# Performance work log

Hardware: AMD Instinct MI355X
Metric: run time of the kernel (lower is better)

## Reference

```python
import jax, jax.numpy as jnp
import numpy as np

N_STATE = 512
M_IN = 64
P_OUT = 64
BATCH = 32
SEQ = 2048


def setup_inputs() -> dict:
    key = jax.random.key(0)
    k1, k2, k3, k4, k5 = jax.random.split(key, 5)
    u = jax.random.normal(k1, (BATCH, SEQ, M_IN), dtype=jnp.float32)
    # CompanionParam init: a ~ randn * 0.01 (keeps companion matrix stable, near shift matrix)
    a = jax.random.normal(k2, (N_STATE,), dtype=jnp.float32) * 0.01
    B = jax.random.normal(k3, (N_STATE, M_IN), dtype=jnp.float32) * 0.05
    C = jax.random.normal(k4, (P_OUT, N_STATE), dtype=jnp.float32) * 0.05
    D = jax.random.normal(k5, (P_OUT, M_IN), dtype=jnp.float32) * 0.05
    return {"u": u, "a": a, "B": B, "C": C, "D": D}


def companion_matrix(a):
    # A[i+1, i] = 1 on subdiagonal; last column = -flip(a)  (matches CompanionParam.matrix)
    n = a.shape[0]
    idx = jnp.arange(n - 1)
    A = jnp.zeros((n, n), dtype=a.dtype)
    A = A.at[idx + 1, idx].set(1.0)
    A = A.at[:, n - 1].set(-a[::-1])
    return A


def reference(u, a, B, C, D):
    # LTI SSM recurrence: x_t = A x_{t-1} + B u_t ; y_t = C x_t + D u_t
    A = companion_matrix(a)  # (n, n)
    batch, T, m = u.shape
    n = a.shape[0]
    u_t = jnp.transpose(u, (1, 0, 2))  # (T, batch, m)
    Bu = jnp.einsum('tbm,nm->tbn', u_t, B)  # precompute input drive (T, batch, n)

    def step(x, bu):
        x_new = x @ A.T + bu  # (batch, n)
        return x_new, x_new

    x0 = jnp.zeros((batch, n), dtype=u.dtype)
    _, xs = jax.lax.scan(step, x0, Bu)  # xs: (T, batch, n)
    ys = jnp.einsum('tbn,pn->tbp', xs, C) + jnp.einsum('tbm,pm->tbp', u_t, D)
    return jnp.transpose(ys, (1, 0, 2))  # (batch, T, p)
```

## Files before the change

### kernel.cpp

```cpp
#include <hip/hip_runtime.h>

#define SEQ  2048
#define NB   32
#define NS   512
#define MI   64
#define PO   64
#define TB   64
#define NTB  32
#define CH   64
#define NCH  8
#define LDU  72
#define LDD  68
#define SG_LDA 72

typedef __attribute__((ext_vector_type(8))) __bf16 bf16x8;
typedef __attribute__((ext_vector_type(4))) float  floatx4;

__device__ inline unsigned short f2bf(float f) {
    unsigned u = __builtin_bit_cast(unsigned, f);
    u += 0x7fff + ((u >> 16) & 1);
    return (unsigned short)(u >> 16);
}

__global__ void __launch_bounds__(256) prep_all_kernel(
    const float* __restrict__ u, const float* __restrict__ B,
    const float* __restrict__ C, const float* __restrict__ D,
    const float* __restrict__ a,
    unsigned short* __restrict__ ubf, unsigned short* __restrict__ BflatT,
    unsigned short* __restrict__ Bws, unsigned short* __restrict__ Cws,
    unsigned short* __restrict__ Dws, unsigned short* __restrict__ qT) {
    __shared__ float a_ext[1024];
    const int bx = blockIdx.x, tid = threadIdx.x;
    if (bx < 2048) {
        const size_t base = ((size_t)bx * 256 + tid) * 8;
        float4 f0 = *(const float4*)(u + base);
        float4 f1 = *(const float4*)(u + base + 4);
        unsigned short tmp[8];
        tmp[0] = f2bf(f0.x); tmp[1] = f2bf(f0.y); tmp[2] = f2bf(f0.z); tmp[3] = f2bf(f0.w);
        tmp[4] = f2bf(f1.x); tmp[5] = f2bf(f1.y); tmp[6] = f2bf(f1.z); tmp[7] = f2bf(f1.w);
        *(uint4*)(ubf + base) = *(uint4*)&tmp[0];
    } else if (bx < 2560) {
        const int i = bx - 2048;
        for (int r = 0; r < 2; ++r) {
            const int id = tid + r * 256;
            const int j = id >> 3, q8 = (id & 7) * 8;
            unsigned short tmp[8];
            if (i >= j) {
                const float4 f0 = *(const float4*)(B + (size_t)(i - j) * MI + q8);
                const float4 f1 = *(const float4*)(B + (size_t)(i - j) * MI + q8 + 4);
                tmp[0] = f2bf(f0.x); tmp[1] = f2bf(f0.y); tmp[2] = f2bf(f0.z); tmp[3] = f2bf(f0.w);
                tmp[4] = f2bf(f1.x); tmp[5] = f2bf(f1.y); tmp[6] = f2bf(f1.z); tmp[7] = f2bf(f1.w);
            } else {
#pragma unroll
                for (int z = 0; z < 8; ++z) tmp[z] = 0;
            }
            *(uint4*)(BflatT + (size_t)i * 4096 + j * 64 + q8) = *(uint4*)&tmp[0];
        }
    } else if (bx < 2624) {
        const int p = bx - 2560;
        for (int x = tid; x < 1024; x += 256) a_ext[x] = (x < NS) ? a[x] : 0.f;
        __syncthreads();
        const int j0 = tid, j1 = tid + 256;
        float acc0 = 0.f, acc1 = 0.f;
        const float4* crow = (const float4*)(C + (size_t)p * NS);
        for (int i4 = 0; i4 < NS / 4; ++i4) {
            const float4 cv = crow[i4];
            const int base = 511 - i4 * 4;
            acc0 += cv.x * a_ext[base + j0]     + cv.y * a_ext[base - 1 + j0] +
                    cv.z * a_ext[base - 2 + j0] + cv.w * a_ext[base - 3 + j0];
            acc1 += cv.x * a_ext[base + j1]     + cv.y * a_ext[base - 1 + j1] +
                    cv.z * a_ext[base - 2 + j1] + cv.w * a_ext[base - 3 + j1];
        }
        qT[(size_t)p * NS + j0] = f2bf(acc0);
        qT[(size_t)p * NS + j1] = f2bf(acc1);
    } else {
        const int idx = (bx - 2624) * 256 + tid;
        const int nB = NS * MI, nC = PO * NS, nD = PO * MI;
        if (idx < nB) Bws[idx] = f2bf(B[idx]);
        else if (idx < nB + nC) Cws[idx - nB] = f2bf(C[idx - nB]);
        else if (idx < nB + nC + nD) Dws[idx - nB - nC] = f2bf(D[idx - nB - nC]);
    }
}

__global__ void __launch_bounds__(256) sgemm_kernel(const unsigned short* __restrict__ ubf,
                                                    const unsigned short* __restrict__ BflatT,
                                                    float* __restrict__ Sbuf) {
    __shared__ unsigned short A_l[4 * 64 * SG_LDA];
    __shared__ unsigned short U_l[4 * 32 * SG_LDA];
    const int ib = blockIdx.x, b = blockIdx.y;
    const int tid = threadIdx.x, lane = tid & 63, w = tid >> 6;
    const int row16 = lane & 15, quad = lane >> 4;
    const int i0 = ib * 64;
    floatx4 acc[2];
#pragma unroll
    for (int ns = 0; ns < 2; ++ns) acc[ns] = (floatx4){0.f, 0.f, 0.f, 0.f};

    for (int jg = 0; jg < 16; ++jg) {
#pragma unroll
        for (int r = 0; r < 8; ++r) {
            const int id = tid + r * 256;
            const int row = id >> 5;
            const int jj = (id >> 3) & 3, q8 = (id & 7) * 8;
            const int j = jg * 4 + jj;
            *(uint4*)&A_l[(jj * 64 + row) * SG_LDA + q8] =
                *(const uint4*)(BflatT + (size_t)(i0 + row) * 4096 + j * 64 + q8);
        }
#pragma unroll
        for (int r = 0; r < 4; ++r) {
            const int id = tid + r * 256;
            const int n = id >> 5;
            const int jj = (id >> 3) & 3, q8 = (id & 7) * 8;
            const int j = jg * 4 + jj;
            *(uint4*)&U_l[(jj * 32 + n) * SG_LDA + q8] =
                *(const uint4*)(ubf + ((size_t)b * SEQ + n * 64 + 63 - j) * MI + q8);
        }
        __syncthreads();
#pragma unroll
        for (int jj = 0; jj < 4; ++jj) {
#pragma unroll
            for (int mk = 0; mk < 2; ++mk) {
                const bf16x8 av = *(const bf16x8*)
                    &A_l[(jj * 64 + w * 16 + row16) * SG_LDA + mk * 32 + quad * 8];
#pragma unroll
                for (int ns = 0; ns < 2; ++ns) {
                    const bf16x8 bv = *(const bf16x8*)
                        &U_l[(jj * 32 + ns * 16 + row16) * SG_LDA + mk * 32 + quad * 8];
                    acc[ns] = __builtin_amdgcn_mfma_f32_16x16x32_bf16(av, bv, acc[ns], 0, 0, 0);
                }
            }
        }
        __syncthreads();
    }
#pragma unroll
    for (int ns = 0; ns < 2; ++ns) {
        const int n = ns * 16 + row16;
        float* dst = Sbuf + ((size_t)b * NTB + n) * NS + i0 + w * 16 + quad * 4;
        *(floatx4*)dst = acc[ns];
    }
}

__global__ void __launch_bounds__(1024) scan_himp_kernel(const float* __restrict__ Sbuf,
                                                         float* __restrict__ Rbuf,
                                                         const float* __restrict__ a,
                                                         float* __restrict__ hbuf) {
    __shared__ __align__(16) char smem[24576];
    const int tid = threadIdx.x;
    if (blockIdx.x < NB) {
        const int b = blockIdx.x;
        const float4* S4 = (const float4*)(Sbuf + (size_t)b * NTB * NS);
        float4* R4 = (float4*)(Rbuf + (size_t)b * NTB * NS);
        for (int o = tid; o < NTB * NS / 4; o += 1024) {
            const int k = o >> 7;
            const int i4 = o & 127;
            float4 acc = make_float4(0.f, 0.f, 0.f, 0.f);
#pragma unroll
            for (int m = 0; m < 8; ++m) {
                if (m <= k - 1 && i4 >= 16 * m) {
                    const float4 s = S4[(k - 1 - m) * 128 + i4 - 16 * m];
                    acc.x += s.x; acc.y += s.y; acc.z += s.z; acc.w += s.w;
                }
            }
            R4[o] = acc;
        }
    } else {
        float* a_l     = (float*)smem;
        float* h_ext   = (float*)(smem + 2560);
        float* part    = (float*)(smem + 12800);
        float* rhs_ext = (float*)(smem + 20992);
        const int kk = tid & 63, grp = tid >> 6;

        for (int x = tid; x < 640; x += 1024) a_l[x] = (x < NS) ? a[x] : 0.f;
        for (int x = tid; x < 640; x += 1024) h_ext[x] = 0.f;
        if (tid < 256) rhs_ext[tid] = 0.f;
        __syncthreads();

        float aw[34];
#pragma unroll
        for (int i = 0; i < 34; ++i) aw[i] = a_l[2 * kk + grp * 32 + i];

        if (tid < 64) {
            if (tid == 0) h_ext[512] = 1.f;
            float acc = (tid >= 1) ? a_l[tid - 1] : 0.f;
            for (int s = 1; s < 64; ++s) {
                const float hs = -__shfl(acc, s);
                if (tid == s) h_ext[512 + s] = hs;
                const float av = a_l[(tid > s) ? (tid - 1 - s) : 0];
                acc += (tid > s) ? av * hs : 0.f;
            }
        }
        __syncthreads();

        int t0 = 64;
        while (t0 < SEQ) {
            float acc0 = 0.f, acc1 = 0.f;
#pragma unroll
            for (int m = 0; m < 8; ++m) {
                const float4 hv = *(const float4*)&h_ext[512 + t0 - grp * 32 - 4 - 4 * m];
                acc0 += aw[4 * m + 0] * hv.w + aw[4 * m + 1] * hv.z +
                        aw[4 * m + 2] * hv.y + aw[4 * m + 3] * hv.x;
                acc1 += aw[4 * m + 1] * hv.w + aw[4 * m + 2] * hv.z +
                        aw[4 * m + 3] * hv.y + aw[4 * m + 4] * hv.x;
            }
            *(float2*)&part[grp * 128 + 2 * kk] = make_float2(acc0, acc1);
            __syncthreads();
            if (tid < 128) {
                float r = 0.f;
#pragma unroll
                for (int g = 0; g < 16; ++g) r += part[g * 128 + tid];
                rhs_ext[128 + tid] = -r;
            }
            __syncthreads();
            {
                const int g = tid >> 7, out = tid & 127;
                const int k0 = g * 16;
                float s = 0.f;
#pragma unroll
                for (int k4 = 0; k4 < 4; ++k4) {
                    const float4 h4 = *(const float4*)&h_ext[512 + k0 + 4 * k4];
                    const int base = 128 + out - k0 - 4 * k4;
                    s += h4.x * rhs_ext[base]     + h4.y * rhs_ext[base - 1] +
                         h4.z * rhs_ext[base - 2] + h4.w * rhs_ext[base - 3];
                }
                part[g * 128 + out] = s;
            }
            __syncthreads();
            if (tid < 128) {
                float r = 0.f;
#pragma unroll
                for (int g = 0; g < 8; ++g) r += part[g * 128 + tid];
                h_ext[512 + t0 + tid] = r;
            }
            __syncthreads();
            t0 += (t0 == 64) ? 64 : 128;
        }
        for (int i = tid; i < SEQ; i += 1024) hbuf[i] = h_ext[512 + i];
    }
}

__global__ void __launch_bounds__(256, 4) ytile_kernel(
    const unsigned short* __restrict__ ubf, const unsigned short* __restrict__ Bws,
    const unsigned short* __restrict__ Cws, const unsigned short* __restrict__ Dws,
    const float* __restrict__ Rbuf, float* __restrict__ fbuf, float* __restrict__ y) {
    __shared__ __align__(16) float buDiag[TB * LDD];
    __shared__ __align__(16) unsigned short Gb[TB * LDU];

    const int blk = blockIdx.x, b = blockIdx.y;
    const int t0 = blk * TB;
    const int tid = threadIdx.x;
    const int lane = tid & 63, w = tid >> 6;
    const int row16 = lane & 15, quad = lane >> 4;
    const size_t rbase = ((size_t)b * NTB + blk) * NS;

    const int dd = lane >> 2, seg = lane & 3;
    const int d  = w * 16 + dd;
    const int tsplit = 63 - d, gseg = tsplit >> 4, jsplit = tsplit & 15;
    const int qb = lane & 60;

    float sA = (d >= 1) ? Rbuf[rbase + d - 1] : 0.f;
    float cB = 0.f;

    floatx4 accY[4];
#pragma unroll
    for (int nt = 0; nt < 4; ++nt) accY[nt] = (floatx4){0.f, 0.f, 0.f, 0.f};

    bf16x8 ufr0[4], ufr1[4];
#pragma unroll
    for (int nt = 0; nt < 4; ++nt) {
        const size_t ub = ((size_t)b * SEQ + t0 + nt * 16 + row16) * MI;
        ufr0[nt] = *(const bf16x8*)(ubf + ub + quad * 8);
        ufr1[nt] = *(const bf16x8*)(ubf + ub + 32 + quad * 8);
    }

    for (int ch = 0; ch < NCH; ++ch) {
        float sA_next = 0.f;
        if (ch + 1 < NCH) sA_next = Rbuf[rbase + (ch + 1) * 64 + d - 1];

        const bf16x8 bf0 = *(const bf16x8*)(Bws + (size_t)(ch * CH + w * 16 + row16) * MI + quad * 8);
        const bf16x8 bf1 = *(const bf16x8*)(Bws + (size_t)(ch * CH + w * 16 + row16) * MI + 32 + quad * 8);
        const bf16x8 cf0 = *(const bf16x8*)(Cws + (size_t)(w * 16 + row16) * NS + ch * CH + quad * 8);
        const bf16x8 cf1 = *(const bf16x8*)(Cws + (size_t)(w * 16 + row16) * NS + ch * CH + 32 + quad * 8);

#pragma unroll
        for (int nt = 0; nt < 4; ++nt) {
            floatx4 dacc = {0.f, 0.f, 0.f, 0.f};
            dacc = __builtin_amdgcn_mfma_f32_16x16x32_bf16(bf0, ufr0[nt], dacc, 0, 0, 0);
            dacc = __builtin_amdgcn_mfma_f32_16x16x32_bf16(bf1, ufr1[nt], dacc, 0, 0, 0);
            const int t = nt * 16 + row16;
            const int ibase = w * 16 + quad * 4;
#pragma unroll
            for (int r = 0; r < 4; ++r) {
                const int dscat = (ibase + r - t) & 63;
                buDiag[dscat * LDD + t] = dacc[r];
            }
        }
        __syncthreads();

        {
            const float* rowp = &buDiag[d * LDD + seg * 16];
            const float4 v0 = *(const float4*)(rowp + 0);
            const float4 v1 = *(const float4*)(rowp + 4);
            const float4 v2 = *(const float4*)(rowp + 8);
            const float4 v3 = *(const float4*)(rowp + 12);
            float pv[16];
            pv[0]  = v0.x;          pv[1]  = pv[0]  + v0.y;
            pv[2]  = pv[1]  + v0.z; pv[3]  = pv[2]  + v0.w;
            pv[4]  = pv[3]  + v1.x; pv[5]  = pv[4]  + v1.y;
            pv[6]  = pv[5]  + v1.z; pv[7]  = pv[6]  + v1.w;
            pv[8]  = pv[7]  + v2.x; pv[9]  = pv[8]  + v2.y;
            pv[10] = pv[9]  + v2.z; pv[11] = pv[10] + v2.w;
            pv[12] = pv[11] + v3.x; pv[13] = pv[12] + v3.y;
            pv[14] = pv[13] + v3.z; pv[15] = pv[14] + v3.w;
            const float total = pv[15];
            const float tq0 = __shfl(total, qb + 0);
            const float tq1 = __shfl(total, qb + 1);
            const float tq2 = __shfl(total, qb + 2);
            const float off = (seg > 0 ? tq0 : 0.f) + (seg > 1 ? tq1 : 0.f) +
                              (seg > 2 ? tq2 : 0.f);
            float plocal = pv[0];
#pragma unroll
            for (int j = 1; j < 16; ++j) plocal = (j == jsplit) ? pv[j] : plocal;
            const float Ps = __shfl(off + plocal, qb + gseg);
            const float exitv = sA + Ps;
            const float baseLo = sA, baseHi = cB - Ps;
#pragma unroll
            for (int j = 0; j < 16; ++j) {
                const int t = seg * 16 + j;
                const float outv = ((t <= tsplit) ? baseLo : baseHi) + off + pv[j];
                Gb[t * LDU + ((d + t) & 63)] = f2bf(outv);
            }
            if (ch == NCH - 1) {
                if (seg == 0) fbuf[(size_t)b * SEQ + t0 + tsplit] = exitv;
            }
            cB = exitv;
            sA = sA_next;
        }
        __syncthreads();

#pragma unroll
        for (int nt = 0; nt < 4; ++nt) {
            const int t = nt * 16 + row16;
            bf16x8 g0 = *(const bf16x8*)&Gb[t * LDU + quad * 8];
            bf16x8 g1 = *(const bf16x8*)&Gb[t * LDU + 32 + quad * 8];
            accY[nt] = __builtin_amdgcn_mfma_f32_16x16x32_bf16(cf0, g0, accY[nt], 0, 0, 0);
            accY[nt] = __builtin_amdgcn_mfma_f32_16x16x32_bf16(cf1, g1, accY[nt], 0, 0, 0);
        }
    }

    const bf16x8 df0 = *(const bf16x8*)(Dws + (size_t)(w * 16 + row16) * MI + quad * 8);
    const bf16x8 df1 = *(const bf16x8*)(Dws + (size_t)(w * 16 + row16) * MI + 32 + quad * 8);
#pragma unroll
    for (int nt = 0; nt < 4; ++nt) {
        const int t = nt * 16 + row16;
        accY[nt] = __builtin_amdgcn_mfma_f32_16x16x32_bf16(df0, ufr0[nt], accY[nt], 0, 0, 0);
        accY[nt] = __builtin_amdgcn_mfma_f32_16x16x32_bf16(df1, ufr1[nt], accY[nt], 0, 0, 0);
        const int p0 = w * 16 + quad * 4;
        *(floatx4*)(y + ((size_t)b * SEQ + t0 + t) * PO + p0) = accY[nt];
    }
}

__global__ void __launch_bounds__(256) sconv_kernel(const float* __restrict__ fbuf,
                                                    const float* __restrict__ hbuf,
                                                    float* __restrict__ sbuf) {
    __shared__ __align__(16) float f_l[64 + SEQ];
    __shared__ __align__(16) float h_lc[SEQ + 8];
    __shared__ __align__(16) float part[16][TB];
    const int blk = blockIdx.x, b = blockIdx.y, tid = threadIdx.x;
    const int t0 = blk * TB;
    const int len = t0 + TB;
    {
        const float4* fs = (const float4*)(fbuf + (size_t)b * SEQ);
        const float4* hs = (const float4*)hbuf;
        float4* f4 = (float4*)f_l;
        float4* h4p = (float4*)h_lc;
        if (tid < 16) f4[tid] = make_float4(0.f, 0.f, 0.f, 0.f);
        for (int i = tid; i < len / 4; i += 256) f4[16 + i] = fs[i];
        const int nh4 = len / 4 + 2;
        for (int i = tid; i < nh4; i += 256)
            h4p[i] = (i < SEQ / 4) ? hs[i] : make_float4(0.f, 0.f, 0.f, 0.f);
    }
    __syncthreads();
    const int o4 = (tid & 15) * 4, grp = tid >> 4;
    const int tb4 = t0 + o4;
    float a0 = 0.f, a1 = 0.f, a2 = 0.f, a3 = 0.f;
    for (int j4 = grp * 4; j4 <= tb4 + 3; j4 += 64) {
        const float4 hv = *(const float4*)&h_lc[j4];
        const int A = tb4 - j4;
        const float4 q0 = *(const float4*)&f_l[60 + A];
        const float4 q1 = *(const float4*)&f_l[64 + A];
        a0 += hv.x * q1.x + hv.y * q0.w + hv.z * q0.z + hv.w * q0.y;
        a1 += hv.x * q1.y + hv.y * q1.x + hv.z * q0.w + hv.w * q0.z;
        a2 += hv.x * q1.z + hv.y * q1.y + hv.z * q1.x + hv.w * q0.w;
        a3 += hv.x * q1.w + hv.y * q1.z + hv.z * q1.y + hv.w * q1.x;
    }
    *(float4*)&part[grp][o4] = make_float4(a0, a1, a2, a3);
    __syncthreads();
    if (tid < TB) {
        float r = 0.f;
#pragma unroll
        for (int g = 0; g < 16; ++g) r += part[g][tid];
        sbuf[(size_t)b * SEQ + t0 + tid] = r;
    }
}

__global__ void __launch_bounds__(256) corr_kernel(
    const float* __restrict__ sbuf, const unsigned short* __restrict__ qT,
    float* __restrict__ y) {
    __shared__ float s_l[NS + TB];
    __shared__ unsigned short Sw[2][TB * LDU];
    const int blk = blockIdx.x, b = blockIdx.y, tid = threadIdx.x;
    const int t0 = blk * TB;
    const int lane = tid & 63, w = tid >> 6;
    const int row16 = lane & 15, quad = lane >> 4;
    for (int idx = tid; idx < NS + TB; idx += 256) {
        const int t = t0 - NS + idx;
        s_l[idx] = (t >= 0) ? sbuf[(size_t)b * SEQ + t] : 0.f;
    }
    floatx4 acc[4];
#pragma unroll
    for (int nt = 0; nt < 4; ++nt) acc[nt] = (floatx4){0.f, 0.f, 0.f, 0.f};
    __syncthreads();

    for (int ch = 0; ch < NCH; ++ch) {
        const int buf = ch & 1;
        const bf16x8 qf0 = *(const bf16x8*)(qT + (size_t)(w * 16 + row16) * NS + ch * CH + quad * 8);
        const bf16x8 qf1 = *(const bf16x8*)(qT + (size_t)(w * 16 + row16) * NS + ch * CH + 32 + quad * 8);
        {
            const int r = tid >> 2, c0 = (tid & 3) * 16;
            unsigned short tmp[16];
            const int base = 511 + r - ch * CH - c0;
#pragma unroll
            for (int jj = 0; jj < 16; ++jj) tmp[jj] = f2bf(s_l[base - jj]);
            *(uint4*)&Sw[buf][r * LDU + c0]     = *(uint4*)&tmp[0];
            *(uint4*)&Sw[buf][r * LDU + c0 + 8] = *(uint4*)&tmp[8];
        }
        __syncthreads();
#pragma unroll
        for (int nt = 0; nt < 4; ++nt) {
            const int t = nt * 16 + row16;
            bf16x8 s0 = *(const bf16x8*)&Sw[buf][t * LDU + quad * 8];
            bf16x8 s1 = *(const bf16x8*)&Sw[buf][t * LDU + 32 + quad * 8];
            acc[nt] = __builtin_amdgcn_mfma_f32_16x16x32_bf16(qf0, s0, acc[nt], 0, 0, 0);
            acc[nt] = __builtin_amdgcn_mfma_f32_16x16x32_bf16(qf1, s1, acc[nt], 0, 0, 0);
        }
    }
#pragma unroll
    for (int nt = 0; nt < 4; ++nt) {
        const int t = nt * 16 + row16;
        const int p0 = w * 16 + quad * 4;
        float* yp = y + ((size_t)b * SEQ + t0 + t) * PO + p0;
        floatx4 old = *(const floatx4*)yp;
        *(floatx4*)yp = old - acc[nt];
    }
}

extern "C" void kernel_launch(void* const* d_in, const int* in_sizes, int n_in,
                              void* d_out, int out_size, void* d_ws,
                              size_t ws_size, hipStream_t stream) {
    const float* u  = (const float*)d_in[0];
    const float* a  = (const float*)d_in[1];
    const float* B  = (const float*)d_in[2];
    const float* Cm = (const float*)d_in[3];
    const float* Dm = (const float*)d_in[4];
    float* y = (float*)d_out;

    char* ws = (char*)d_ws;
    unsigned short* Bws = (unsigned short*)ws;                  ws += NS * MI * 2;
    unsigned short* Cws = (unsigned short*)ws;                  ws += PO * NS * 2;
    unsigned short* Dws = (unsigned short*)ws;                  ws += PO * MI * 2;
    unsigned short* qTw = (unsigned short*)ws;                  ws += PO * NS * 2;
    unsigned short* ubf = (unsigned short*)ws;                  ws += (size_t)NB * SEQ * MI * 2;
    unsigned short* Bft = (unsigned short*)ws;                  ws += (size_t)NS * 4096 * 2;
    float* Sbuf = (float*)ws;                                   ws += (size_t)NB * NTB * NS * 4;
    float* Rbuf = (float*)ws;                                   ws += (size_t)NB * NTB * NS * 4;
    float* fbuf = (float*)ws;                                   ws += (size_t)NB * SEQ * 4;
    float* sbuf = (float*)ws;                                   ws += (size_t)NB * SEQ * 4;
    float* hbuf = (float*)ws;

    prep_all_kernel<<<dim3(2896), dim3(256), 0, stream>>>(
        u, B, Cm, Dm, a, ubf, Bft, Bws, Cws, Dws, qTw);
    sgemm_kernel<<<dim3(8, 32), dim3(256), 0, stream>>>(ubf, Bft, Sbuf);
    scan_himp_kernel<<<dim3(NB + 1), dim3(1024), 0, stream>>>(Sbuf, Rbuf, a, hbuf);
    ytile_kernel<<<dim3(NTB, NB), dim3(256), 0, stream>>>(
        ubf, Bws, Cws, Dws, Rbuf, fbuf, y);
    sconv_kernel<<<dim3(NTB, NB), dim3(256), 0, stream>>>(fbuf, hbuf, sbuf);
    corr_kernel<<<dim3(NTB, NB), dim3(256), 0, stream>>>(sbuf, qTw, y);
}
```

Before: 204.0 us.

## Fold scan kernel into prep and ytile, drop Rbuf round trip

The h-impulse recurrence moves into an extra 1024-thread block of the prep kernel, so it runs alongside the conversions, and prep switches to 1024-thread blocks. The Rbuf prefix-sum pass is dropped: each ytile block now builds its own seed vector in shared memory from Sbuf. This removes one kernel launch and the Rbuf global write and read. The corr kernel now stores s as bf16 in shared memory, converting once instead of on every reuse. In exchange, the h-scan block now shares a launch with many short blocks and could lengthen the prep kernel's tail, and ytile takes on redundant seed summation.

```diff
diff --git a/kernel.cpp b/kernel.cpp
--- a/kernel.cpp
+++ b/kernel.cpp
@@ -22,63 +22,132 @@
     return (unsigned short)(u >> 16);
 }
 
-__global__ void __launch_bounds__(256) prep_all_kernel(
+__global__ void __launch_bounds__(1024) prep_all_kernel(
     const float* __restrict__ u, const float* __restrict__ B,
     const float* __restrict__ C, const float* __restrict__ D,
     const float* __restrict__ a,
     unsigned short* __restrict__ ubf, unsigned short* __restrict__ BflatT,
     unsigned short* __restrict__ Bws, unsigned short* __restrict__ Cws,
-    unsigned short* __restrict__ Dws, unsigned short* __restrict__ qT) {
-    __shared__ float a_ext[1024];
+    unsigned short* __restrict__ Dws, unsigned short* __restrict__ qT,
+    float* __restrict__ hbuf) {
+    __shared__ __align__(16) char smem[24576];
     const int bx = blockIdx.x, tid = threadIdx.x;
-    if (bx < 2048) {
-        const size_t base = ((size_t)bx * 256 + tid) * 8;
+    if (bx < 512) {
+        const size_t base = ((size_t)bx * 1024 + tid) * 8;
         float4 f0 = *(const float4*)(u + base);
         float4 f1 = *(const float4*)(u + base + 4);
         unsigned short tmp[8];
         tmp[0] = f2bf(f0.x); tmp[1] = f2bf(f0.y); tmp[2] = f2bf(f0.z); tmp[3] = f2bf(f0.w);
         tmp[4] = f2bf(f1.x); tmp[5] = f2bf(f1.y); tmp[6] = f2bf(f1.z); tmp[7] = f2bf(f1.w);
         *(uint4*)(ubf + base) = *(uint4*)&tmp[0];
-    } else if (bx < 2560) {
-        const int i = bx - 2048;
-        for (int r = 0; r < 2; ++r) {
-            const int id = tid + r * 256;
-            const int j = id >> 3, q8 = (id & 7) * 8;
-            unsigned short tmp[8];
-            if (i >= j) {
-                const float4 f0 = *(const float4*)(B + (size_t)(i - j) * MI + q8);
-                const float4 f1 = *(const float4*)(B + (size_t)(i - j) * MI + q8 + 4);
-                tmp[0] = f2bf(f0.x); tmp[1] = f2bf(f0.y); tmp[2] = f2bf(f0.z); tmp[3] = f2bf(f0.w);
-                tmp[4] = f2bf(f1.x); tmp[5] = f2bf(f1.y); tmp[6] = f2bf(f1.z); tmp[7] = f2bf(f1.w);
-            } else {
-#pragma unroll
-                for (int z = 0; z < 8; ++z) tmp[z] = 0;
-            }
-            *(uint4*)(BflatT + (size_t)i * 4096 + j * 64 + q8) = *(uint4*)&tmp[0];
-        }
-    } else if (bx < 2624) {
-        const int p = bx - 2560;
-        for (int x = tid; x < 1024; x += 256) a_ext[x] = (x < NS) ? a[x] : 0.f;
-        __syncthreads();
-        const int j0 = tid, j1 = tid + 256;
-        float acc0 = 0.f, acc1 = 0.f;
+    } else if (bx < 768) {
+        const int i = (bx - 512) * 2 + (tid >> 9);
+        const int id = tid & 511;
+        const int j = id >> 3, q8 = (id & 7) * 8;
+        unsigned short tmp[8];
+        if (i >= j) {
+            const float4 f0 = *(const float4*)(B + (size_t)(i - j) * MI + q8);
+            const float4 f1 = *(const float4*)(B + (size_t)(i - j) * MI + q8 + 4);
+            tmp[0] = f2bf(f0.x); tmp[1] = f2bf(f0.y); tmp[2] = f2bf(f0.z); tmp[3] = f2bf(f0.w);
+            tmp[4] = f2bf(f1.x); tmp[5] = f2bf(f1.y); tmp[6] = f2bf(f1.z); tmp[7] = f2bf(f1.w);
+        } else {
+#pragma unroll
+            for (int z = 0; z < 8; ++z) tmp[z] = 0;
+        }
+        *(uint4*)(BflatT + (size_t)i * 4096 + j * 64 + q8) = *(uint4*)&tmp[0];
+    } else if (bx < 800) {
+        float* a_ext = (float*)smem;
+        const int p = (bx - 768) * 2 + (tid >> 9);
+        const int j0 = tid & 511;
+        a_ext[tid] = (tid < NS) ? a[tid] : 0.f;
+        __syncthreads();
+        float acc0 = 0.f;
         const float4* crow = (const float4*)(C + (size_t)p * NS);
         for (int i4 = 0; i4 < NS / 4; ++i4) {
             const float4 cv = crow[i4];
             const int base = 511 - i4 * 4;
             acc0 += cv.x * a_ext[base + j0]     + cv.y * a_ext[base - 1 + j0] +
                     cv.z * a_ext[base - 2 + j0] + cv.w * a_ext[base - 3 + j0];
-            acc1 += cv.x * a_ext[base + j1]     + cv.y * a_ext[base - 1 + j1] +
-                    cv.z * a_ext[base - 2 + j1] + cv.w * a_ext[base - 3 + j1];
         }
         qT[(size_t)p * NS + j0] = f2bf(acc0);
-        qT[(size_t)p * NS + j1] = f2bf(acc1);
-    } else {
-        const int idx = (bx - 2624) * 256 + tid;
+    } else if (bx < 868) {
+        const int idx = (bx - 800) * 1024 + tid;
         const int nB = NS * MI, nC = PO * NS, nD = PO * MI;
         if (idx < nB) Bws[idx] = f2bf(B[idx]);
         else if (idx < nB + nC) Cws[idx - nB] = f2bf(C[idx - nB]);
         else if (idx < nB + nC + nD) Dws[idx - nB - nC] = f2bf(D[idx - nB - nC]);
+    } else {
+        float* a_l     = (float*)smem;
+        float* h_ext   = (float*)(smem + 2560);
+        float* part    = (float*)(smem + 12800);
+        float* rhs_ext = (float*)(smem + 20992);
+        const int kk = tid & 63, grp = tid >> 6;
+
+        for (int x = tid; x < 640; x += 1024) a_l[x] = (x < NS) ? a[x] : 0.f;
+        for (int x = tid; x < 640; x += 1024) h_ext[x] = 0.f;
+        if (tid < 256) rhs_ext[tid] = 0.f;
+        __syncthreads();
+
+        float aw[34];
+#pragma unroll
+        for (int i = 0; i < 34; ++i) aw[i] = a_l[2 * kk + grp * 32 + i];
+
+        if (tid < 64) {
+            if (tid == 0) h_ext[512] = 1.f;
+            float acc = (tid >= 1) ? a_l[tid - 1] : 0.f;
+            for (int s = 1; s < 64; ++s) {
+                const float hs = -__shfl(acc, s);
+                if (tid == s) h_ext[512 + s] = hs;
+                const float av = a_l[(tid > s) ? (tid - 1 - s) : 0];
+                acc += (tid > s) ? av * hs : 0.f;
+            }
+        }
+        __syncthreads();
+
+        int t0 = 64;
+        while (t0 < SEQ) {
+            float acc0 = 0.f, acc1 = 0.f;
+#pragma unroll
+            for (int m = 0; m < 8; ++m) {
+                const float4 hv = *(const float4*)&h_ext[512 + t0 - grp * 32 - 4 - 4 * m];
+                acc0 += aw[4 * m + 0] * hv.w + aw[4 * m + 1] * hv.z +
+                        aw[4 * m + 2] * hv.y + aw[4 * m + 3] * hv.x;
+                acc1 += aw[4 * m + 1] * hv.w + aw[4 * m + 2] * hv.z +
+                        aw[4 * m + 3] * hv.y + aw[4 * m + 4] * hv.x;
+            }
+            *(float2*)&part[grp * 128 + 2 * kk] = make_float2(acc0, acc1);
+            __syncthreads();
+            if (tid < 128) {
+                float r = 0.f;
+#pragma unroll
+                for (int g = 0; g < 16; ++g) r += part[g * 128 + tid];
+                rhs_ext[128 + tid] = -r;
+            }
+            __syncthreads();
+            {
+                const int g = tid >> 7, out = tid & 127;
+                const int k0 = g * 16;
+                float s = 0.f;
+#pragma unroll
+                for (int k4 = 0; k4 < 4; ++k4) {
+                    const float4 h4 = *(const float4*)&h_ext[512 + k0 + 4 * k4];
+                    const int base = 128 + out - k0 - 4 * k4;
+                    s += h4.x * rhs_ext[base]     + h4.y * rhs_ext[base - 1] +
+                         h4.z * rhs_ext[base - 2] + h4.w * rhs_ext[base - 3];
+                }
+                part[g * 128 + out] = s;
+            }
+            __syncthreads();
+            if (tid < 128) {
+                float r = 0.f;
+#pragma unroll
+                for (int g = 0; g < 8; ++g) r += part[g * 128 + tid];
+                h_ext[512 + t0 + tid] = r;
+            }
+            __syncthreads();
+            t0 += (t0 == 64) ? 64 : 128;
+        }
+        for (int i = tid; i < SEQ; i += 1024) hbuf[i] = h_ext[512 + i];
     }
 }
 
@@ -139,124 +208,41 @@
     }
 }
 
-__global__ void __launch_bounds__(1024) scan_himp_kernel(const float* __restrict__ Sbuf,
-                                                         float* __restrict__ Rbuf,
-                                                         const float* __restrict__ a,
-                                                         float* __restrict__ hbuf) {
-    __shared__ __align__(16) char smem[24576];
-    const int tid = threadIdx.x;
-    if (blockIdx.x < NB) {
-        const int b = blockIdx.x;
-        const float4* S4 = (const float4*)(Sbuf + (size_t)b * NTB * NS);
-        float4* R4 = (float4*)(Rbuf + (size_t)b * NTB * NS);
-        for (int o = tid; o < NTB * NS / 4; o += 1024) {
-            const int k = o >> 7;
-            const int i4 = o & 127;
-            float4 acc = make_float4(0.f, 0.f, 0.f, 0.f);
-#pragma unroll
-            for (int m = 0; m < 8; ++m) {
-                if (m <= k - 1 && i4 >= 16 * m) {
-                    const float4 s = S4[(k - 1 - m) * 128 + i4 - 16 * m];
-                    acc.x += s.x; acc.y += s.y; acc.z += s.z; acc.w += s.w;
-                }
-            }
-            R4[o] = acc;
-        }
-    } else {
-        float* a_l     = (float*)smem;
-        float* h_ext   = (float*)(smem + 2560);
-        float* part    = (float*)(smem + 12800);
-        float* rhs_ext = (float*)(smem + 20992);
-        const int kk = tid & 63, grp = tid >> 6;
-
-        for (int x = tid; x < 640; x += 1024) a_l[x] = (x < NS) ? a[x] : 0.f;
-        for (int x = tid; x < 640; x += 1024) h_ext[x] = 0.f;
-        if (tid < 256) rhs_ext[tid] = 0.f;
-        __syncthreads();
-
-        float aw[34];
-#pragma unroll
-        for (int i = 0; i < 34; ++i) aw[i] = a_l[2 * kk + grp * 32 + i];
-
-        if (tid < 64) {
-            if (tid == 0) h_ext[512] = 1.f;
-            float acc = (tid >= 1) ? a_l[tid - 1] : 0.f;
-            for (int s = 1; s < 64; ++s) {
-                const float hs = -__shfl(acc, s);
-                if (tid == s) h_ext[512 + s] = hs;
-                const float av = a_l[(tid > s) ? (tid - 1 - s) : 0];
-                acc += (tid > s) ? av * hs : 0.f;
-            }
-        }
-        __syncthreads();
-
-        int t0 = 64;
-        while (t0 < SEQ) {
-            float acc0 = 0.f, acc1 = 0.f;
-#pragma unroll
-            for (int m = 0; m < 8; ++m) {
-                const float4 hv = *(const float4*)&h_ext[512 + t0 - grp * 32 - 4 - 4 * m];
-                acc0 += aw[4 * m + 0] * hv.w + aw[4 * m + 1] * hv.z +
-                        aw[4 * m + 2] * hv.y + aw[4 * m + 3] * hv.x;
-                acc1 += aw[4 * m + 1] * hv.w + aw[4 * m + 2] * hv.z +
-                        aw[4 * m + 3] * hv.y + aw[4 * m + 4] * hv.x;
-            }
-            *(float2*)&part[grp * 128 + 2 * kk] = make_float2(acc0, acc1);
-            __syncthreads();
-            if (tid < 128) {
-                float r = 0.f;
-#pragma unroll
-                for (int g = 0; g < 16; ++g) r += part[g * 128 + tid];
-                rhs_ext[128 + tid] = -r;
-            }
-            __syncthreads();
-            {
-                const int g = tid >> 7, out = tid & 127;
-                const int k0 = g * 16;
-                float s = 0.f;
-#pragma unroll
-                for (int k4 = 0; k4 < 4; ++k4) {
-                    const float4 h4 = *(const float4*)&h_ext[512 + k0 + 4 * k4];
-                    const int base = 128 + out - k0 - 4 * k4;
-                    s += h4.x * rhs_ext[base]     + h4.y * rhs_ext[base - 1] +
-                         h4.z * rhs_ext[base - 2] + h4.w * rhs_ext[base - 3];
-                }
-                part[g * 128 + out] = s;
-            }
-            __syncthreads();
-            if (tid < 128) {
-                float r = 0.f;
-#pragma unroll
-                for (int g = 0; g < 8; ++g) r += part[g * 128 + tid];
-                h_ext[512 + t0 + tid] = r;
-            }
-            __syncthreads();
-            t0 += (t0 == 64) ? 64 : 128;
-        }
-        for (int i = tid; i < SEQ; i += 1024) hbuf[i] = h_ext[512 + i];
-    }
-}
-
 __global__ void __launch_bounds__(256, 4) ytile_kernel(
     const unsigned short* __restrict__ ubf, const unsigned short* __restrict__ Bws,
     const unsigned short* __restrict__ Cws, const unsigned short* __restrict__ Dws,
-    const float* __restrict__ Rbuf, float* __restrict__ fbuf, float* __restrict__ y) {
+    const float* __restrict__ Sbuf, float* __restrict__ fbuf, float* __restrict__ y) {
     __shared__ __align__(16) float buDiag[TB * LDD];
     __shared__ __align__(16) unsigned short Gb[TB * LDU];
+    __shared__ float seedL[NS];
 
     const int blk = blockIdx.x, b = blockIdx.y;
     const int t0 = blk * TB;
     const int tid = threadIdx.x;
     const int lane = tid & 63, w = tid >> 6;
     const int row16 = lane & 15, quad = lane >> 4;
-    const size_t rbase = ((size_t)b * NTB + blk) * NS;
 
     const int dd = lane >> 2, seg = lane & 3;
     const int d  = w * 16 + dd;
     const int tsplit = 63 - d, gseg = tsplit >> 4, jsplit = tsplit & 15;
     const int qb = lane & 60;
 
-    float sA = (d >= 1) ? Rbuf[rbase + d - 1] : 0.f;
+    {
+        const int mtop = (blk - 1 < 7) ? (blk - 1) : 7;
+#pragma unroll
+        for (int half = 0; half < 2; ++half) {
+            const int s = tid + half * 256;
+            float sd = 0.f;
+            if (s >= 1) {
+                const int i = s - 1, q = i >> 6, r = i & 63;
+                const int mmax = (mtop < q) ? mtop : q;
+                for (int m = 0; m <= mmax; ++m)
+                    sd += Sbuf[((size_t)b * NTB + (blk - 1 - m)) * NS + (q - m) * 64 + r];
+            }
+            seedL[s] = sd;
+        }
+    }
+
     float cB = 0.f;
 
     floatx4 accY[4];
@@ -272,9 +258,6 @@
     }
 
     for (int ch = 0; ch < NCH; ++ch) {
-        float sA_next = 0.f;
-        if (ch + 1 < NCH) sA_next = Rbuf[rbase + (ch + 1) * 64 + d - 1];
-
         const bf16x8 bf0 = *(const bf16x8*)(Bws + (size_t)(ch * CH + w * 16 + row16) * MI + quad * 8);
         const bf16x8 bf1 = *(const bf16x8*)(Bws + (size_t)(ch * CH + w * 16 + row16) * MI + 32 + quad * 8);
         const bf16x8 cf0 = *(const bf16x8*)(Cws + (size_t)(w * 16 + row16) * NS + ch * CH + quad * 8);
@@ -296,6 +279,7 @@
         __syncthreads();
 
         {
+            const float sA = seedL[ch * CH + d];
             const float* rowp = &buDiag[d * LDD + seg * 16];
             const float4 v0 = *(const float4*)(rowp + 0);
             const float4 v1 = *(const float4*)(rowp + 4);
@@ -332,7 +316,6 @@
                 if (seg == 0) fbuf[(size_t)b * SEQ + t0 + tsplit] = exitv;
             }
             cB = exitv;
-            sA = sA_next;
         }
         __syncthreads();
 
@@ -405,7 +388,7 @@
 __global__ void __launch_bounds__(256) corr_kernel(
     const float* __restrict__ sbuf, const unsigned short* __restrict__ qT,
     float* __restrict__ y) {
-    __shared__ float s_l[NS + TB];
+    __shared__ unsigned short s_bf[NS + TB];
     __shared__ unsigned short Sw[2][TB * LDU];
     const int blk = blockIdx.x, b = blockIdx.y, tid = threadIdx.x;
     const int t0 = blk * TB;
@@ -413,7 +396,7 @@
     const int row16 = lane & 15, quad = lane >> 4;
     for (int idx = tid; idx < NS + TB; idx += 256) {
         const int t = t0 - NS + idx;
-        s_l[idx] = (t >= 0) ? sbuf[(size_t)b * SEQ + t] : 0.f;
+        s_bf[idx] = (t >= 0) ? f2bf(sbuf[(size_t)b * SEQ + t]) : (unsigned short)0;
     }
     floatx4 acc[4];
 #pragma unroll
@@ -429,7 +412,7 @@
             unsigned short tmp[16];
             const int base = 511 + r - ch * CH - c0;
 #pragma unroll
-            for (int jj = 0; jj < 16; ++jj) tmp[jj] = f2bf(s_l[base - jj]);
+            for (int jj = 0; jj < 16; ++jj) tmp[jj] = s_bf[base - jj];
             *(uint4*)&Sw[buf][r * LDU + c0]     = *(uint4*)&tmp[0];
             *(uint4*)&Sw[buf][r * LDU + c0 + 8] = *(uint4*)&tmp[8];
         }
@@ -471,17 +454,15 @@
     unsigned short* ubf = (unsigned short*)ws;                  ws += (size_t)NB * SEQ * MI * 2;
     unsigned short* Bft = (unsigned short*)ws;                  ws += (size_t)NS * 4096 * 2;
     float* Sbuf = (float*)ws;                                   ws += (size_t)NB * NTB * NS * 4;
-    float* Rbuf = (float*)ws;                                   ws += (size_t)NB * NTB * NS * 4;
     float* fbuf = (float*)ws;                                   ws += (size_t)NB * SEQ * 4;
     float* sbuf = (float*)ws;                                   ws += (size_t)NB * SEQ * 4;
     float* hbuf = (float*)ws;
 
-    prep_all_kernel<<<dim3(2896), dim3(256), 0, stream>>>(
-        u, B, Cm, Dm, a, ubf, Bft, Bws, Cws, Dws, qTw);
+    prep_all_kernel<<<dim3(869), dim3(1024), 0, stream>>>(
+        u, B, Cm, Dm, a, ubf, Bft, Bws, Cws, Dws, qTw, hbuf);
     sgemm_kernel<<<dim3(8, 32), dim3(256), 0, stream>>>(ubf, Bft, Sbuf);
-    scan_himp_kernel<<<dim3(NB + 1), dim3(1024), 0, stream>>>(Sbuf, Rbuf, a, hbuf);
     ytile_kernel<<<dim3(NTB, NB), dim3(256), 0, stream>>>(
-        ubf, Bws, Cws, Dws, Rbuf, fbuf, y);
+        ubf, Bws, Cws, Dws, Sbuf, fbuf, y);
     sconv_kernel<<<dim3(NTB, NB), dim3(256), 0, stream>>>(fbuf, hbuf, sbuf);
     corr_kernel<<<dim3(NTB, NB), dim3(256), 0, stream>>>(sbuf, qTw, y);
 }
```

After: 195.3 us. -4.3%, faster.
